# Performance work log

Measured on AMD Instinct MI355X. Metric: run time of the kernel, lower is better.

The kernel has to match this reference:

```python
import jax, jax.numpy as jnp
import numpy as np
import math

B, TQ, TK, D, H, K = 4, 1024, 1536, 1024, 16, 1
DV = D // H * K  # 64
DP = D * K       # projection dim


def setup_inputs() -> dict:
    key = jax.random.key(0)
    ks = jax.random.split(key, 12)
    s = 0.02
    query = jax.random.normal(ks[0], (B, TQ, D), dtype=jnp.float32)
    key_value = jax.random.normal(ks[1], (B, TK, D), dtype=jnp.float32)
    relative = jax.random.normal(ks[2], (B, TK, D), dtype=jnp.float32)
    # Transformer-XL causal mask: query i may attend to key j <= i + mem
    mem = TK - TQ
    i = jnp.arange(TQ)[:, None]
    j = jnp.arange(TK)[None, :]
    mask = jnp.broadcast_to(j > i + mem, (B, TQ, TK))  # True = masked
    Wq = jax.random.normal(ks[3], (D, DP), dtype=jnp.float32) * s
    Wk = jax.random.normal(ks[4], (D, DP), dtype=jnp.float32) * s
    Wv = jax.random.normal(ks[5], (D, DP), dtype=jnp.float32) * s
    Wr = jax.random.normal(ks[6], (D, DP), dtype=jnp.float32) * s
    Wo = jax.random.normal(ks[7], (DP, D), dtype=jnp.float32) * s
    u = jax.random.normal(ks[8], (DV,), dtype=jnp.float32) * s
    v = jax.random.normal(ks[9], (DV,), dtype=jnp.float32) * s
    gamma = jnp.ones((D,), dtype=jnp.float32)
    beta = jnp.zeros((D,), dtype=jnp.float32)
    return {"query": query, "key_value": key_value, "relative": relative,
            "mask": mask, "Wq": Wq, "Wk": Wk, "Wv": Wv, "Wr": Wr, "Wo": Wo,
            "u": u, "v": v, "gamma": gamma, "beta": beta}


def _layer_norm(x, gamma, beta, eps=1e-5):
    mu = jnp.mean(x, axis=-1, keepdims=True)
    var = jnp.mean(jnp.square(x - mu), axis=-1, keepdims=True)
    return (x - mu) * jax.lax.rsqrt(var + eps) * gamma + beta


def reference(query, key_value, relative, mask, Wq, Wk, Wv, Wr, Wo, u, v, gamma, beta):
    b, tq, d = query.shape
    tk = key_value.shape[1]
    dv = u.shape[0]
    h = Wq.shape[1] // dv
    q = (query @ Wq).reshape(b, tq, h, dv)
    k = (key_value @ Wk).reshape(b, tk, h, dv)
    val = (key_value @ Wv).reshape(b, tk, h, dv)
    r = (relative @ Wr).reshape(b, tk, h, dv)
    # content term (q+u)K^T and position term (q+v)R^T, per head
    ac = jnp.einsum('bqhd,bkhd->bhqk', q + u, k)
    bd = jnp.einsum('bqhd,bkhd->bhqk', q + v, r)
    logits = (ac + bd) * (1.0 / math.sqrt(dv))
    logits = jnp.where(mask[:, None, :, :], -jnp.inf, logits)
    w = jax.nn.softmax(logits, axis=-1)
    ctx = jnp.einsum('bhqk,bkhd->bqhd', w, val).reshape(b, tq, h * dv)
    out = ctx @ Wo + query  # residual
    return _layer_norm(out, gamma, beta)
```

## Files before the change

### kernel.cpp

```cpp
#include <hip/hip_runtime.h>


typedef unsigned short u16;
typedef __attribute__((ext_vector_type(8))) short short8;
typedef __attribute__((ext_vector_type(4))) float floatx4;

__device__ __forceinline__ float bf2f(u16 u) {
    union { unsigned int i; float f; } w; w.i = ((unsigned int)u) << 16; return w.f;
}
__device__ __forceinline__ u16 f2bf(float f) {
    union { unsigned int i; float f; } w; w.f = f;
    unsigned int u = w.i;
    return (u16)((u + 0x7FFFu + ((u >> 16) & 1u)) >> 16);
}

__device__ __forceinline__ void gl_lds16(const u16* g, u16* lds) {
    __builtin_amdgcn_global_load_lds(
        (const __attribute__((address_space(1))) void*)g,
        (__attribute__((address_space(3))) void*)lds, 16, 0, 0);
}

__global__ __launch_bounds__(256) void cvt3_kernel(
    const float* __restrict__ x0, u16* __restrict__ y0, int n0,
    const float* __restrict__ x1, u16* __restrict__ y1, int n1,
    const float* __restrict__ x2, u16* __restrict__ y2, int n2)
{
    const int which = blockIdx.y;
    const float* x = (which == 0) ? x0 : (which == 1) ? x1 : x2;
    u16* y         = (which == 0) ? y0 : (which == 1) ? y1 : y2;
    const int n    = (which == 0) ? n0 : (which == 1) ? n1 : n2;
    const int i = (blockIdx.x * 256 + threadIdx.x) * 8;
    if (i >= n) return;
    float4 a = *(const float4*)&x[i];
    float4 b = *(const float4*)&x[i + 4];
    short8 o;
    o[0] = (short)f2bf(a.x); o[1] = (short)f2bf(a.y);
    o[2] = (short)f2bf(a.z); o[3] = (short)f2bf(a.w);
    o[4] = (short)f2bf(b.x); o[5] = (short)f2bf(b.y);
    o[6] = (short)f2bf(b.z); o[7] = (short)f2bf(b.w);
    *(short8*)&y[i] = o;
}

__global__ __launch_bounds__(256) void transpose5_kernel(
    const float* __restrict__ Wq, const float* __restrict__ Wk,
    const float* __restrict__ Wr, const float* __restrict__ Wv,
    const float* __restrict__ Wo,
    u16* __restrict__ WqT, u16* __restrict__ WkrT,
    u16* __restrict__ WvT, u16* __restrict__ WoT)
{
    const int z = blockIdx.z;
    const float* W; u16* WT; int dst_ld, dst_koff;
    switch (z) {
        case 0: W = Wq; WT = WqT;  dst_ld = 1024; dst_koff = 0;    break;
        case 1: W = Wk; WT = WkrT; dst_ld = 2048; dst_koff = 0;    break;
        case 2: W = Wr; WT = WkrT; dst_ld = 2048; dst_koff = 1024; break;
        case 3: W = Wv; WT = WvT;  dst_ld = 1024; dst_koff = 0;    break;
        default:W = Wo; WT = WoT;  dst_ld = 1024; dst_koff = 0;    break;
    }
    __shared__ u16 ts[64][72];
    const int k0 = blockIdx.x * 64, n0 = blockIdx.y * 64;
    const int r  = threadIdx.x >> 2;
    const int c4 = (threadIdx.x & 3) << 4;
    const float* src = &W[(size_t)(k0 + r) * 1024 + n0 + c4];
    for (int j = 0; j < 16; j += 4) {
        float4 a = *(const float4*)(src + j);
        ts[r][c4 + j + 0] = f2bf(a.x);
        ts[r][c4 + j + 1] = f2bf(a.y);
        ts[r][c4 + j + 2] = f2bf(a.z);
        ts[r][c4 + j + 3] = f2bf(a.w);
    }
    __syncthreads();
    short8 t0, t1;
    for (int j = 0; j < 8; j++) t0[j] = (short)ts[c4 + j][r];
    for (int j = 0; j < 8; j++) t1[j] = (short)ts[c4 + 8 + j][r];
    u16* dst = &WT[(size_t)(n0 + r) * dst_ld + dst_koff + k0 + c4];
    *(short8*)dst       = t0;
    *(short8*)(dst + 8) = t1;
}

__global__ __launch_bounds__(256) void wuv_kernel(
    const float* __restrict__ Wk, const float* __restrict__ Wr,
    const float* __restrict__ u, const float* __restrict__ v,
    u16* __restrict__ wuvb)
{
    int idx = blockIdx.x * 256 + threadIdx.x;
    int c = idx >> 4, h = idx & 15;
    float au = 0.f, av = 0.f;
    for (int d = 0; d < 64; d++) {
        au += Wk[(size_t)c * 1024 + h * 64 + d] * u[d];
        av += Wr[(size_t)c * 1024 + h * 64 + d] * v[d];
    }
    wuvb[h * 2048 + c]        = f2bf(au);
    wuvb[h * 2048 + 1024 + c] = f2bf(av);
}

template <int EPI>
__device__ __forceinline__ void gemm_body(
    const u16* __restrict__ A0, const u16* __restrict__ A1,
    const u16* __restrict__ WT, void* __restrict__ out,
    int Kld, int kbeg, int kend, int Ksplit, int T,
    int bm, int bn, u16* As, u16* Ws)
{
    const int tid = threadIdx.x;
    const int wave = tid >> 6, lane = tid & 63;
    const int wm = wave >> 1, wn = wave & 1;
    const int l16 = lane & 15, quad = lane >> 4;

    floatx4 acc[4][4];
    const floatx4 zf = {0.f, 0.f, 0.f, 0.f};
    for (int i = 0; i < 4; i++) for (int j = 0; j < 4; j++) acc[i][j] = zf;

    const int m_base = bm * 128, n_base = bn * 128;
    const int rl = lane >> 2;
    const int cl = (lane & 3) * 8;

    for (int k0 = kbeg; k0 < kend; k0 += 32) {
        const u16* Aptr; int kk;
        if (k0 < Ksplit) { Aptr = A0; kk = k0; } else { Aptr = A1; kk = k0 - Ksplit; }
        __syncthreads();
        for (int half = 0; half < 2; half++) {
            const int r = wave * 32 + half * 16;
            gl_lds16(Aptr + (size_t)(m_base + r + rl) * 1024 + kk + cl, &As[r * 32]);
            gl_lds16(WT   + (size_t)(n_base + r + rl) * Kld  + k0 + cl, &Ws[r * 32]);
        }
        __syncthreads();

        short8 af[4], bf[4];
        for (int i = 0; i < 4; i++) {
            af[i] = *(const short8*)&As[(wm * 64 + i * 16 + l16) * 32 + quad * 8];
            bf[i] = *(const short8*)&Ws[(wn * 64 + i * 16 + l16) * 32 + quad * 8];
        }
        for (int i = 0; i < 4; i++)
            for (int j = 0; j < 4; j++)
                acc[i][j] = __builtin_amdgcn_mfma_f32_16x16x32_bf16(af[i], bf[j], acc[i][j], 0, 0, 0);
    }

    for (int i = 0; i < 4; i++) {
        for (int rg = 0; rg < 4; rg++) {
            const int m = m_base + wm * 64 + i * 16 + quad * 4 + rg;
            float* op = (float*)out;
            for (int j = 0; j < 4; j++) {
                const int col = n_base + wn * 64 + j * 16 + l16;
                op[(size_t)m * 1024 + col] = acc[i][j][rg];
            }
        }
    }
}

__device__ __forceinline__ void stage_half(
    const u16* __restrict__ src, int src_ld, int row_base, int col_base,
    u16* lds_slot, int wave, int lane)
{
    const int r = wave * 16 + (lane >> 2);
    const int c = (((lane & 3) ^ ((lane >> 2) & 3)) << 3);
    gl_lds16(src + (size_t)(row_base + r) * src_ld + col_base + c,
             lds_slot + wave * 512);
    gl_lds16(src + (size_t)(row_base + 128 + r) * src_ld + col_base + c,
             lds_slot + 4096 + wave * 512);
}

template <int EPI, int T>
__device__ __forceinline__ void gemm256_body(
    const u16* __restrict__ A0, const u16* __restrict__ A1,
    const u16* __restrict__ WT, void* __restrict__ out,
    int Kld, int NT, int KsplitTile, int bm, int bn,
    u16* As, u16* Bs)
{
    const int tid  = threadIdx.x;
    const int wave = tid >> 6, lane = tid & 63;
    const int wm = wave >> 2, wn = wave & 3;
    const int l16 = lane & 15, quad = lane >> 4;
    const int m_base = bm * 256, n_base = bn * 256;

    floatx4 acc[8][4];
    const floatx4 zf = {0.f, 0.f, 0.f, 0.f};
    #pragma unroll
    for (int i = 0; i < 8; i++)
        #pragma unroll
        for (int j = 0; j < 4; j++) acc[i][j] = zf;

    {
        const u16* sa0 = (0 < KsplitTile) ? A0 : A1;
        stage_half(sa0, 1024, m_base, 0,  As + 0 * 8192, wave, lane);
        stage_half(WT,  Kld,  n_base, 0,  Bs + 0 * 8192, wave, lane);
        stage_half(sa0, 1024, m_base, 32, As + 1 * 8192, wave, lane);
        stage_half(WT,  Kld,  n_base, 32, Bs + 1 * 8192, wave, lane);
        const u16* sa1 = (1 < KsplitTile) ? A0 : A1;
        const int  c1  = (1 < KsplitTile) ? 64 : (1 - KsplitTile) * 64;
        stage_half(sa1, 1024, m_base, c1, As + 2 * 8192, wave, lane);
        stage_half(WT,  Kld,  n_base, 64, Bs + 2 * 8192, wave, lane);
    }

    for (int t = 0; t < NT; ++t) {
        if (t + 1 < NT) asm volatile("s_waitcnt vmcnt(4)" ::: "memory");
        else            asm volatile("s_waitcnt vmcnt(0)" ::: "memory");
        __builtin_amdgcn_s_barrier();

        short8 bfr[4];
        #pragma unroll
        for (int ph = 0; ph < 4; ++ph) {
            if (ph) __builtin_amdgcn_s_barrier();
            const int ks = ph >> 1, mh = ph & 1;

            if (ph == 0) {
                if (t + 1 < NT) {
                    const int tt = t + 1;
                    const u16* sa = (tt < KsplitTile) ? A0 : A1;
                    const int cb = (tt < KsplitTile ? tt : tt - KsplitTile) * 64 + 32;
                    stage_half(sa, 1024, m_base, cb, As + ((2 * tt + 1) & 3) * 8192, wave, lane);
                }
            } else if (ph == 1) {
                if (t + 1 < NT)
                    stage_half(WT, Kld, n_base, (t + 1) * 64 + 32,
                               Bs + ((2 * (t + 1) + 1) & 3) * 8192, wave, lane);
            } else if (ph == 2) {
                if (t + 2 < NT) {
                    const int tt = t + 2;
                    const u16* sa = (tt < KsplitTile) ? A0 : A1;
                    const int cb = (tt < KsplitTile ? tt : tt - KsplitTile) * 64;
                    stage_half(sa, 1024, m_base, cb, As + ((2 * tt) & 3) * 8192, wave, lane);
                }
            } else {
                if (t + 2 < NT)
                    stage_half(WT, Kld, n_base, (t + 2) * 64,
                               Bs + ((2 * (t + 2)) & 3) * 8192, wave, lane);
            }

            const u16* Aslot = As + ((2 * t + ks) & 3) * 8192;
            const u16* Bslot = Bs + ((2 * t + ks) & 3) * 8192;
            if (mh == 0) {
                #pragma unroll
                for (int nj = 0; nj < 4; ++nj) {
                    const int row = wn * 64 + nj * 16 + l16;
                    bfr[nj] = *(const short8*)&Bslot[row * 32 + (((quad ^ row) & 3) << 3)];
                }
            }
            short8 af[4];
            #pragma unroll
            for (int mi = 0; mi < 4; ++mi) {
                const int row = wm * 128 + mh * 64 + mi * 16 + l16;
                af[mi] = *(const short8*)&Aslot[row * 32 + (((quad ^ row) & 3) << 3)];
            }

            __builtin_amdgcn_s_setprio(1);
            #pragma unroll
            for (int mi = 0; mi < 4; ++mi)
                #pragma unroll
                for (int nj = 0; nj < 4; ++nj)
                    acc[mh * 4 + mi][nj] = __builtin_amdgcn_mfma_f32_16x16x32_bf16(
                        af[mi], bfr[nj], acc[mh * 4 + mi][nj], 0, 0, 0);
            __builtin_amdgcn_s_setprio(0);
        }
    }

    u16* op = (u16*)out;
    #pragma unroll
    for (int mi = 0; mi < 8; ++mi) {
        #pragma unroll
        for (int rg = 0; rg < 4; ++rg) {
            const int m = m_base + wm * 128 + mi * 16 + quad * 4 + rg;
            const int b = m / T, tk = m % T;
            #pragma unroll
            for (int nj = 0; nj < 4; ++nj) {
                const int col = n_base + wn * 64 + nj * 16 + l16;
                const int h = col >> 6, d = col & 63;
                if (EPI == 0) {
                    op[(((size_t)(b * 16 + h) * T + tk) << 6) + d] = f2bf(acc[mi][nj][rg]);
                } else {
                    op[((size_t)(b * 16 + h) * 64 + d) * 1536 + tk] = f2bf(acc[mi][nj][rg]);
                }
            }
        }
    }
}

__device__ __forceinline__ void bias_body8(
    const u16* __restrict__ kvb, const u16* __restrict__ relb,
    const u16* __restrict__ wuvb, float* __restrict__ bias, int bblk)
{
    const int tid = threadIdx.x;
    const int wave = tid >> 6, lane = tid & 63;
    const int l16 = lane & 15, quad = lane >> 4;
    const int tBase = bblk * 128 + wave * 16;

    floatx4 acc = {0.f, 0.f, 0.f, 0.f};
    const u16* arow_kv  = kvb  + (size_t)(tBase + l16) * 1024;
    const u16* arow_rel = relb + (size_t)(tBase + l16) * 1024;
    const u16* brow     = wuvb + (size_t)l16 * 2048;

    for (int ks = 0; ks < 64; ks++) {
        const int k0 = ks * 32;
        const u16* ap = (k0 < 1024) ? (arow_kv + k0) : (arow_rel + k0 - 1024);
        short8 af = *(const short8*)(ap + quad * 8);
        short8 bf = *(const short8*)(brow + k0 + quad * 8);
        acc = __builtin_amdgcn_mfma_f32_16x16x32_bf16(af, bf, acc, 0, 0, 0);
    }
    for (int rg = 0; rg < 4; rg++) {
        const int tg = tBase + quad * 4 + rg;
        const int b = tg / 1536, t = tg % 1536;
        bias[((size_t)b * 16 + l16) * 1536 + t] = acc[rg];
    }
}

__global__ __launch_bounds__(512) void fused_proj_v2(
    const u16* __restrict__ qb, const u16* __restrict__ kvb,
    const u16* __restrict__ relb,
    const u16* __restrict__ WqT, const u16* __restrict__ WkrT,
    const u16* __restrict__ WvT, const u16* __restrict__ wuvb,
    u16* __restrict__ Qh, u16* __restrict__ KRh, u16* __restrict__ Vt,
    float* __restrict__ bias)
{
    __shared__ __align__(128) u16 As[4 * 256 * 32];
    __shared__ __align__(128) u16 Bs[4 * 256 * 32];
    const int blk = blockIdx.x;
    if (blk < 96) {
        gemm256_body<0, 1536>(kvb, relb, WkrT, KRh, 2048, 32, 16,
                              blk % 24, blk / 24, As, Bs);
    } else if (blk < 192) {
        const int i = blk - 96;
        gemm256_body<2, 1536>(kvb, kvb, WvT, Vt, 1024, 16, 99,
                              i % 24, i / 24, As, Bs);
    } else if (blk < 256) {
        const int i = blk - 192;
        gemm256_body<0, 1024>(qb, qb, WqT, Qh, 1024, 16, 99,
                              i % 16, i / 16, As, Bs);
    } else {
        bias_body8(kvb, relb, wuvb, bias, blk - 256);
    }
}

__global__ __launch_bounds__(256) void out_gemm(
    const u16* __restrict__ ctx, const u16* __restrict__ WoT,
    float* __restrict__ outp)
{
    __shared__ u16 smem[2 * 128 * 32];
    const int z = blockIdx.z;
    gemm_body<3>(ctx, nullptr, WoT,
                 outp + (size_t)z * 4 * 1024 * 1024, 1024,
                 z * 512, z * 512 + 512, 1024, 1024,
                 blockIdx.x, blockIdx.y, smem, smem + 128 * 32);
}

__global__ __launch_bounds__(256) void attn_kernel(
    const u16* __restrict__ Qh,
    const u16* __restrict__ KRh,
    const u16* __restrict__ Vt,
    const float* __restrict__ bias,
    u16* __restrict__ ctx)
{
    const int blk  = blockIdx.x;
    const int hb   = blk & 63;
    const int qblk = blk >> 6;
    const int b = hb >> 4, h = hb & 15;
    const int tid = threadIdx.x;
    const int wave = tid >> 6, lane = tid & 63;
    const int l16 = lane & 15, quad = lane >> 4;
    const int q0 = qblk * 128;

    const u16* Qp = Qh  + (size_t)hb * 1024 * 64;
    const u16* Kp = KRh + (size_t)hb * 1536 * 64;
    const u16* Vp = Vt  + (size_t)hb * 64 * 1536;
    const float* bp = bias + (size_t)hb * 1536;

    __shared__ u16 Ps[4][2][16][68];

    short8 aq[2][2];
    for (int mi = 0; mi < 2; mi++)
        for (int ks = 0; ks < 2; ks++)
            aq[mi][ks] = *(const short8*)
                &Qp[(size_t)(q0 + wave * 32 + mi * 16 + l16) * 64 + ks * 32 + quad * 8];

    const floatx4 zf = {0.f, 0.f, 0.f, 0.f};
    floatx4 accO[2][4];
    float lsum[2][4];
    for (int mi = 0; mi < 2; mi++)
        for (int j = 0; j < 4; j++) accO[mi][j] = zf;
    for (int mi = 0; mi < 2; mi++)
        for (int rg = 0; rg < 4; rg++) lsum[mi][rg] = 0.f;

    const int nkt = 2 * qblk + 10;
    for (int kt = 0; kt < nkt; kt++) {
        const int k0 = kt * 64;

        short8 bk[4][2], bv[4][2];
        float bcol[4];
        for (int n = 0; n < 4; n++)
            for (int ks = 0; ks < 2; ks++)
                bk[n][ks] = *(const short8*)
                    &Kp[(size_t)(k0 + n * 16 + l16) * 64 + ks * 32 + quad * 8];
        for (int j = 0; j < 4; j++)
            for (int ks = 0; ks < 2; ks++)
                bv[j][ks] = *(const short8*)
                    &Vp[(size_t)(j * 16 + l16) * 1536 + k0 + ks * 32 + quad * 8];
        for (int n = 0; n < 4; n++) bcol[n] = bp[k0 + n * 16 + l16];

        const bool domask = (k0 + 63 > q0 + 512);

        for (int mi = 0; mi < 2; mi++) {
            floatx4 accS[4];
            for (int n = 0; n < 4; n++) {
                accS[n] = zf;
                for (int ks = 0; ks < 2; ks++)
                    accS[n] = __builtin_amdgcn_mfma_f32_16x16x32_bf16(
                        aq[mi][ks], bk[n][ks], accS[n], 0, 0, 0);
            }
            const int qrow = q0 + wave * 32 + mi * 16 + quad * 4;
            for (int n = 0; n < 4; n++) {
                const int col = k0 + n * 16 + l16;
                for (int rg = 0; rg < 4; rg++) {
                    float s = (accS[n][rg] + bcol[n]) * 0.125f;
                    if (domask && col > qrow + rg + 512) s = -1e30f;
                    const float p = __expf(s);
                    lsum[mi][rg] += p;
                    Ps[wave][mi][quad * 4 + rg][n * 16 + l16] = f2bf(p);
                }
            }
            short8 ap[2];
            for (int ks = 0; ks < 2; ks++)
                ap[ks] = *(const short8*)&Ps[wave][mi][l16][ks * 32 + quad * 8];
            for (int j = 0; j < 4; j++)
                for (int ks = 0; ks < 2; ks++)
                    accO[mi][j] = __builtin_amdgcn_mfma_f32_16x16x32_bf16(
                        ap[ks], bv[j][ks], accO[mi][j], 0, 0, 0);
        }
    }

    for (int mi = 0; mi < 2; mi++)
        for (int rg = 0; rg < 4; rg++) {
            float s = lsum[mi][rg];
            for (int off = 1; off < 16; off <<= 1) s += __shfl_xor(s, off, 64);
            lsum[mi][rg] = s;
        }

    for (int mi = 0; mi < 2; mi++)
        for (int j = 0; j < 4; j++)
            for (int rg = 0; rg < 4; rg++) {
                const int q = q0 + wave * 32 + mi * 16 + quad * 4 + rg;
                const int d = j * 16 + l16;
                ctx[((size_t)b * 1024 + q) * 1024 + h * 64 + d] =
                    f2bf(accO[mi][j][rg] / lsum[mi][rg]);
            }
}

__global__ __launch_bounds__(256) void ln_kernel(
    const float* __restrict__ x0, const float* __restrict__ x1,
    const float* __restrict__ q,
    const float* __restrict__ gamma, const float* __restrict__ beta,
    float* __restrict__ out)
{
    const int row = blockIdx.x;
    const int tid = threadIdx.x;
    const size_t base = (size_t)row * 1024 + tid * 4;
    float4 a = *(const float4*)&x0[base];
    float4 c = *(const float4*)&x1[base];
    float4 r = *(const float4*)&q[base];
    float4 v;
    v.x = a.x + c.x + r.x; v.y = a.y + c.y + r.y;
    v.z = a.z + c.z + r.z; v.w = a.w + c.w + r.w;
    float s  = v.x + v.y + v.z + v.w;
    float ss = v.x * v.x + v.y * v.y + v.z * v.z + v.w * v.w;
    for (int off = 1; off < 64; off <<= 1) {
        s  += __shfl_xor(s, off, 64);
        ss += __shfl_xor(ss, off, 64);
    }
    __shared__ float sm[8];
    const int wave = tid >> 6, lane = tid & 63;
    if (lane == 0) { sm[wave] = s; sm[4 + wave] = ss; }
    __syncthreads();
    s  = sm[0] + sm[1] + sm[2] + sm[3];
    ss = sm[4] + sm[5] + sm[6] + sm[7];
    const float mu  = s * (1.f / 1024.f);
    const float var = ss * (1.f / 1024.f) - mu * mu;
    const float inv = rsqrtf(var + 1e-5f);
    float* op = out + (size_t)row * 1024;
    const float* ve = &v.x;
    for (int j = 0; j < 4; j++) {
        const int c2 = tid * 4 + j;
        op[c2] = (ve[j] - mu) * inv * gamma[c2] + beta[c2];
    }
}

extern "C" void kernel_launch(void* const* d_in, const int* in_sizes, int n_in,
                              void* d_out, int out_size, void* d_ws, size_t ws_size,
                              hipStream_t stream)
{
    const float* query     = (const float*)d_in[0];
    const float* key_value = (const float*)d_in[1];
    const float* relative  = (const float*)d_in[2];
    const float* Wq = (const float*)d_in[4];
    const float* Wk = (const float*)d_in[5];
    const float* Wv = (const float*)d_in[6];
    const float* Wr = (const float*)d_in[7];
    const float* Wo = (const float*)d_in[8];
    const float* u  = (const float*)d_in[9];
    const float* v  = (const float*)d_in[10];
    const float* gamma = (const float*)d_in[11];
    const float* beta  = (const float*)d_in[12];

    char* wsp = (char*)d_ws;
    auto alloc = [&](size_t bytes) -> char* {
        char* p = wsp; wsp += (bytes + 255) & ~(size_t)255; return p;
    };
    u16*   qb   = (u16*)alloc((size_t)4 * 1024 * 1024 * 2);
    u16*   kvb  = (u16*)alloc((size_t)4 * 1536 * 1024 * 2);
    u16*   relb = (u16*)alloc((size_t)4 * 1536 * 1024 * 2);
    u16*   WqT  = (u16*)alloc((size_t)1024 * 1024 * 2);
    u16*   WkrT = (u16*)alloc((size_t)1024 * 2048 * 2);
    u16*   WvT  = (u16*)alloc((size_t)1024 * 1024 * 2);
    u16*   WoT  = (u16*)alloc((size_t)1024 * 1024 * 2);
    u16*   wuvb = (u16*)alloc((size_t)16 * 2048 * 2);
    u16*   Qh   = (u16*)alloc((size_t)4 * 16 * 1024 * 64 * 2);
    u16*   KRh  = (u16*)alloc((size_t)4 * 16 * 1536 * 64 * 2);
    u16*   Vt   = (u16*)alloc((size_t)4 * 16 * 64 * 1536 * 2);
    float* bias = (float*)alloc((size_t)4 * 16 * 1536 * 4);
    u16*   ctx  = (u16*)alloc((size_t)4 * 1024 * 1024 * 2);
    float* outp = (float*)alloc((size_t)2 * 4 * 1024 * 1024 * 4);

    const dim3 tb(256);
    cvt3_kernel<<<dim3(3072, 3), tb, 0, stream>>>(
        query, qb, 4 * 1024 * 1024,
        key_value, kvb, 4 * 1536 * 1024,
        relative, relb, 4 * 1536 * 1024);

    transpose5_kernel<<<dim3(16, 16, 5), tb, 0, stream>>>(
        Wq, Wk, Wr, Wv, Wo, WqT, WkrT, WvT, WoT);
    wuv_kernel<<<64, tb, 0, stream>>>(Wk, Wr, u, v, wuvb);

    fused_proj_v2<<<dim3(304), dim3(512), 0, stream>>>(
        qb, kvb, relb, WqT, WkrT, WvT, wuvb, Qh, KRh, Vt, bias);

    attn_kernel<<<dim3(512), tb, 0, stream>>>(Qh, KRh, Vt, bias, ctx);

    out_gemm<<<dim3(32, 8, 2), tb, 0, stream>>>(ctx, WoT, outp);
    ln_kernel<<<4096, tb, 0, stream>>>(
        outp, outp + (size_t)4 * 1024 * 1024, query, gamma, beta, (float*)d_out);
}
```

Before: 336.6 us.

## Split attention key range across wave pairs and use exp2 with transposed score MFMA

Attention blocks now cover 64 query rows with two waves per query sub-block, each handling alternating key tiles. Partial outputs and row sums are combined through shared memory, and the grid doubles to 1024 blocks to raise parallelism and occupancy. Scores are computed transposed so each lane owns one query row, which allows a float4 bias load, packed bf16 conversion and cheaper row-sum reductions. Scaling is folded into a log2e constant so v_exp_f32 can be used directly. The cost is an extra LDS reduction and a block-wide sync at the end.

```diff
diff --git a/kernel.cpp b/kernel.cpp
--- a/kernel.cpp
+++ b/kernel.cpp
@@ -4,6 +4,8 @@
 typedef unsigned short u16;
 typedef __attribute__((ext_vector_type(8))) short short8;
 typedef __attribute__((ext_vector_type(4))) float floatx4;
+
+#define ATTN_SC 0.18033688011112042f
 
 __device__ __forceinline__ float bf2f(u16 u) {
     union { unsigned int i; float f; } w; w.i = ((unsigned int)u) << 16; return w.f;
@@ -298,7 +300,7 @@
     for (int rg = 0; rg < 4; rg++) {
         const int tg = tBase + quad * 4 + rg;
         const int b = tg / 1536, t = tg % 1536;
-        bias[((size_t)b * 16 + l16) * 1536 + t] = acc[rg];
+        bias[((size_t)b * 16 + l16) * 1536 + t] = acc[rg] * ATTN_SC;
     }
 }
 
@@ -341,7 +343,7 @@
                  blockIdx.x, blockIdx.y, smem, smem + 128 * 32);
 }
 
-__global__ __launch_bounds__(256) void attn_kernel(
+__global__ __launch_bounds__(256, 4) void attn_kernel(
     const u16* __restrict__ Qh,
     const u16* __restrict__ KRh,
     const u16* __restrict__ Vt,
@@ -350,96 +352,149 @@
 {
     const int blk  = blockIdx.x;
     const int hb   = blk & 63;
-    const int qblk = blk >> 6;
+    const int qb   = blk >> 6;
     const int b = hb >> 4, h = hb & 15;
     const int tid = threadIdx.x;
     const int wave = tid >> 6, lane = tid & 63;
     const int l16 = lane & 15, quad = lane >> 4;
-    const int q0 = qblk * 128;
+    const int qsub = wave >> 1, khalf = wave & 1;
+    const int q0 = qb * 64 + qsub * 32;
 
     const u16* Qp = Qh  + (size_t)hb * 1024 * 64;
     const u16* Kp = KRh + (size_t)hb * 1536 * 64;
     const u16* Vp = Vt  + (size_t)hb * 64 * 1536;
     const float* bp = bias + (size_t)hb * 1536;
 
-    __shared__ u16 Ps[4][2][16][68];
+    __shared__ u16   Ps[4][2][16][68];
+    __shared__ float Obuf[2][2][16][66];
+    __shared__ float Lbuf[2][2][16];
 
     short8 aq[2][2];
+    #pragma unroll
     for (int mi = 0; mi < 2; mi++)
+        #pragma unroll
         for (int ks = 0; ks < 2; ks++)
             aq[mi][ks] = *(const short8*)
-                &Qp[(size_t)(q0 + wave * 32 + mi * 16 + l16) * 64 + ks * 32 + quad * 8];
+                &Qp[(size_t)(q0 + mi * 16 + l16) * 64 + ks * 32 + quad * 8];
 
     const floatx4 zf = {0.f, 0.f, 0.f, 0.f};
     floatx4 accO[2][4];
-    float lsum[2][4];
+    float lsum[2] = {0.f, 0.f};
+    #pragma unroll
     for (int mi = 0; mi < 2; mi++)
+        #pragma unroll
         for (int j = 0; j < 4; j++) accO[mi][j] = zf;
-    for (int mi = 0; mi < 2; mi++)
-        for (int rg = 0; rg < 4; rg++) lsum[mi][rg] = 0.f;
-
-    const int nkt = 2 * qblk + 10;
-    for (int kt = 0; kt < nkt; kt++) {
+
+    const int nkt = qb + 9;
+    for (int kt = khalf; kt < nkt; kt += 2) {
         const int k0 = kt * 64;
 
         short8 bk[4][2], bv[4][2];
-        float bcol[4];
+        float4 bc[4];
+        #pragma unroll
         for (int n = 0; n < 4; n++)
+            #pragma unroll
             for (int ks = 0; ks < 2; ks++)
                 bk[n][ks] = *(const short8*)
                     &Kp[(size_t)(k0 + n * 16 + l16) * 64 + ks * 32 + quad * 8];
+        #pragma unroll
         for (int j = 0; j < 4; j++)
+            #pragma unroll
             for (int ks = 0; ks < 2; ks++)
                 bv[j][ks] = *(const short8*)
                     &Vp[(size_t)(j * 16 + l16) * 1536 + k0 + ks * 32 + quad * 8];
-        for (int n = 0; n < 4; n++) bcol[n] = bp[k0 + n * 16 + l16];
-
-        const bool domask = (k0 + 63 > q0 + 512);
-
+        #pragma unroll
+        for (int n = 0; n < 4; n++)
+            bc[n] = *(const float4*)&bp[k0 + n * 16 + quad * 4];
+
+        #pragma unroll
         for (int mi = 0; mi < 2; mi++) {
             floatx4 accS[4];
+            #pragma unroll
             for (int n = 0; n < 4; n++) {
                 accS[n] = zf;
+                #pragma unroll
                 for (int ks = 0; ks < 2; ks++)
                     accS[n] = __builtin_amdgcn_mfma_f32_16x16x32_bf16(
-                        aq[mi][ks], bk[n][ks], accS[n], 0, 0, 0);
-            }
-            const int qrow = q0 + wave * 32 + mi * 16 + quad * 4;
+                        bk[n][ks], aq[mi][ks], accS[n], 0, 0, 0);
+            }
+            const int qg = q0 + mi * 16 + l16;
+            const bool domask = (k0 + 63 > q0 + mi * 16 + 512);
+            const int lim = qg + 512 - k0;
+            #pragma unroll
             for (int n = 0; n < 4; n++) {
-                const int col = k0 + n * 16 + l16;
+                const int limn = lim - n * 16 - quad * 4;
+                const float* bcn = (const float*)&bc[n];
+                float pv[4];
+                #pragma unroll
                 for (int rg = 0; rg < 4; rg++) {
-                    float s = (accS[n][rg] + bcol[n]) * 0.125f;
-                    if (domask && col > qrow + rg + 512) s = -1e30f;
-                    const float p = __expf(s);
-                    lsum[mi][rg] += p;
-                    Ps[wave][mi][quad * 4 + rg][n * 16 + l16] = f2bf(p);
+                    float s = fmaf(accS[n][rg], ATTN_SC, bcn[rg]);
+                    if (domask && rg > limn) s = -1e30f;
+                    float pe;
+                    asm("v_exp_f32 %0, %1" : "=v"(pe) : "v"(s));
+                    lsum[mi] += pe;
+                    pv[rg] = pe;
                 }
+                unsigned w0, w1;
+                asm("v_cvt_pk_bf16_f32 %0, %1, %2" : "=v"(w0) : "v"(pv[0]), "v"(pv[1]));
+                asm("v_cvt_pk_bf16_f32 %0, %1, %2" : "=v"(w1) : "v"(pv[2]), "v"(pv[3]));
+                unsigned* pw = (unsigned*)&Ps[wave][mi][l16][n * 16 + quad * 4];
+                pw[0] = w0; pw[1] = w1;
             }
             short8 ap[2];
+            #pragma unroll
             for (int ks = 0; ks < 2; ks++)
                 ap[ks] = *(const short8*)&Ps[wave][mi][l16][ks * 32 + quad * 8];
+            #pragma unroll
             for (int j = 0; j < 4; j++)
+                #pragma unroll
                 for (int ks = 0; ks < 2; ks++)
                     accO[mi][j] = __builtin_amdgcn_mfma_f32_16x16x32_bf16(
                         ap[ks], bv[j][ks], accO[mi][j], 0, 0, 0);
         }
     }
 
-    for (int mi = 0; mi < 2; mi++)
-        for (int rg = 0; rg < 4; rg++) {
-            float s = lsum[mi][rg];
-            for (int off = 1; off < 16; off <<= 1) s += __shfl_xor(s, off, 64);
-            lsum[mi][rg] = s;
-        }
-
-    for (int mi = 0; mi < 2; mi++)
-        for (int j = 0; j < 4; j++)
-            for (int rg = 0; rg < 4; rg++) {
-                const int q = q0 + wave * 32 + mi * 16 + quad * 4 + rg;
-                const int d = j * 16 + l16;
-                ctx[((size_t)b * 1024 + q) * 1024 + h * 64 + d] =
-                    f2bf(accO[mi][j][rg] / lsum[mi][rg]);
-            }
+    #pragma unroll
+    for (int mi = 0; mi < 2; mi++) {
+        float s = lsum[mi];
+        s += __shfl_xor(s, 16, 64);
+        s += __shfl_xor(s, 32, 64);
+        lsum[mi] = s;
+    }
+
+    if (khalf == 1) {
+        #pragma unroll
+        for (int mi = 0; mi < 2; mi++) {
+            #pragma unroll
+            for (int j = 0; j < 4; j++)
+                #pragma unroll
+                for (int rg = 0; rg < 4; rg++)
+                    Obuf[qsub][mi][quad * 4 + rg][j * 16 + l16] = accO[mi][j][rg];
+            if (quad == 0) Lbuf[qsub][mi][l16] = lsum[mi];
+        }
+    }
+    __syncthreads();
+    if (khalf == 0) {
+        #pragma unroll
+        for (int mi = 0; mi < 2; mi++) {
+            const float lt = lsum[mi] + Lbuf[qsub][mi][l16];
+            float ltr[4];
+            #pragma unroll
+            for (int rg = 0; rg < 4; rg++)
+                ltr[rg] = __shfl(lt, quad * 4 + rg, 16);
+            #pragma unroll
+            for (int j = 0; j < 4; j++)
+                #pragma unroll
+                for (int rg = 0; rg < 4; rg++) {
+                    const float o = accO[mi][j][rg]
+                                  + Obuf[qsub][mi][quad * 4 + rg][j * 16 + l16];
+                    const int q = q0 + mi * 16 + quad * 4 + rg;
+                    const int d = j * 16 + l16;
+                    ctx[((size_t)b * 1024 + q) * 1024 + h * 64 + d] =
+                        f2bf(o / ltr[rg]);
+                }
+        }
+    }
 }
 
 __global__ __launch_bounds__(256) void ln_kernel(
@@ -529,7 +584,7 @@
     fused_proj_v2<<<dim3(304), dim3(512), 0, stream>>>(
         qb, kvb, relb, WqT, WkrT, WvT, wuvb, Qh, KRh, Vt, bias);
 
-    attn_kernel<<<dim3(512), tb, 0, stream>>>(Qh, KRh, Vt, bias, ctx);
+    attn_kernel<<<dim3(1024), tb, 0, stream>>>(Qh, KRh, Vt, bias, ctx);
 
     out_gemm<<<dim3(32, 8, 2), tb, 0, stream>>>(ctx, WoT, outp);
     ln_kernel<<<4096, tb, 0, stream>>>(
```

After: 336.9 us. Within noise of the previous version (+0.1%).
